# Kernel tuning notes

Measured on AMD Instinct MI355X. Metric: run time of the kernel, lower is better.

## Reference

```python
import jax, jax.numpy as jnp
import numpy as np

K = 8        # num capsules
DD = 64      # per-capsule dim (delta_d)
D = K * DD   # 512
T = 16384    # num target nodes (segments)
NB = 100000  # num neighbor nodes
E = 131072   # num edges
ROUIT = 3
BETA = 0.5


def seg_softmax(p, seg, num):
    # softmax over entries sharing the same segment id (axis 0)
    m = jax.lax.stop_gradient(jax.ops.segment_max(p, seg, num_segments=num))
    e = jnp.exp(p - m[seg])
    s = jax.ops.segment_sum(e, seg, num_segments=num)
    return e / s[seg]


def l2norm(x):
    # F.normalize along last axis with eps=1e-12
    n = jnp.sqrt(jnp.sum(x * x, axis=-1, keepdims=True))
    return x / jnp.maximum(n, 1e-12)


def setup_inputs() -> dict:
    key = jax.random.key(0)
    ks = jax.random.split(key, 9)
    return {
        "x_nb": jax.random.normal(ks[0], (NB, 512), dtype=jnp.float32),
        "ppr": jax.random.uniform(ks[1], (E,), dtype=jnp.float32),
        "pca_w": jax.random.normal(ks[2], (512, D), dtype=jnp.float32) * 0.02,
        "pca_b": jnp.zeros((D,), dtype=jnp.float32),
        "mlp_w": jax.random.normal(ks[3], (D, 40), dtype=jnp.float32) * 0.02,
        "mlp_b": jnp.zeros((40,), dtype=jnp.float32),
        "row_idx": jnp.sort(jax.random.randint(ks[4], (E,), 0, T, dtype=jnp.int32)),
        "col_idx": jax.random.randint(ks[5], (E,), 0, NB, dtype=jnp.int32),
        "x_idx": jax.random.randint(ks[6], (T,), 0, NB, dtype=jnp.int32),
    }


def reference(x_nb, ppr, pca_w, pca_b, mlp_w, mlp_b, row_idx, col_idx, x_idx):
    # pca projection + relu
    x = jax.nn.relu(x_nb @ pca_w + pca_b)            # (NB, D)
    # segment softmax of ppr over targets
    ppr = seg_softmax(ppr, row_idx, T)               # (E,)
    # is_xNorm: per-capsule l2 normalization
    x = l2norm(x.reshape(-1, K, DD)).reshape(-1, D)
    z = x[col_idx]                                   # (E, D) gathered neighbors
    zk = z.reshape(-1, K, DD)                        # (E, K, DD)
    # init_mtd == 2: ppr-weighted scatter-sum init
    u = jax.ops.segment_sum(z * ppr[:, None], row_idx, num_segments=T)  # (T, D)
    for it in range(ROUIT):
        uk = u[row_idx].reshape(-1, K, DD)           # (E, K, DD)
        p = jnp.einsum('ekd,ekd->ek', uk, zk)        # (E, K) capsule logits
        # attention == 1: segment softmax then blend with ppr
        p = seg_softmax(p, row_idx, T)
        p = BETA * p + (1.0 - BETA) * ppr[:, None]
        # final segment softmax
        p = seg_softmax(p, row_idx, T)
        u = jax.ops.segment_sum(zk * p[:, :, None], row_idx, num_segments=T)  # (T, K, DD)
        if it < ROUIT - 1:
            u = l2norm(u)
        u = u.reshape(T, D)
    out = jax.nn.relu(u)                             # dropout is identity at eval
    logits = out @ mlp_w + mlp_b                     # (T, nclass)
    return jax.nn.log_softmax(logits, axis=1)
```

## Files before the change

kernel.cpp:

```cpp
#include <hip/hip_runtime.h>
#include <cstdint>
#include <cstddef>

#define NB_N 100000
#define E_N  131072
#define T_N  16384
#define D_N  512
#define NCLS 40
#define NTILES 782
#define CAPR 12

typedef unsigned short u16;
typedef unsigned int   u32;
typedef __attribute__((ext_vector_type(8))) short  short8;
typedef __attribute__((ext_vector_type(4))) float  floatx4;

__device__ __forceinline__ u16 f2bf(float f) {
  u32 u = __float_as_uint(f);
  return (u16)((u + 0x7fffu + ((u >> 16) & 1u)) >> 16);
}
__device__ __forceinline__ void unpack8(uint4 z, float* f) {
  f[0] = __uint_as_float(z.x << 16);
  f[1] = __uint_as_float(z.x & 0xffff0000u);
  f[2] = __uint_as_float(z.y << 16);
  f[3] = __uint_as_float(z.y & 0xffff0000u);
  f[4] = __uint_as_float(z.z << 16);
  f[5] = __uint_as_float(z.z & 0xffff0000u);
  f[6] = __uint_as_float(z.w << 16);
  f[7] = __uint_as_float(z.w & 0xffff0000u);
}
__device__ __forceinline__ void gload_lds16(const void* g, void* s) {
  __builtin_amdgcn_global_load_lds(
      (const __attribute__((address_space(1))) unsigned int*)g,
      (__attribute__((address_space(3))) unsigned int*)s, 16, 0, 0);
}
__device__ __forceinline__ u32 cvtpk_bf16(float lo, float hi) {
  u32 r;
  asm("v_cvt_pk_bf16_f32 %0, %1, %2" : "=v"(r) : "v"(lo), "v"(hi));
  return r;
}

__global__ void conv_bt(const float* __restrict__ w, u16* __restrict__ Bt) {
  int i = blockIdx.x * 256 + threadIdx.x;
  int n = i >> 9, k = i & 511;
  Bt[i] = f2bf(w[k * 512 + n]);
}

__global__ void conv_bt2(const float* __restrict__ w, u16* __restrict__ Bt2) {
  int i = blockIdx.x * 256 + threadIdx.x;
  int n = i >> 9, k = i & 511;
  Bt2[i] = (n < NCLS) ? f2bf(w[k * NCLS + n]) : (u16)0;
}

__global__ void build_offs(const int* __restrict__ rowi, int* __restrict__ offs) {
  int e = blockIdx.x * 256 + threadIdx.x;
  if (e >= E_N) return;
  int r  = rowi[e];
  int rp = (e == 0) ? -1 : rowi[e - 1];
  for (int t = rp + 1; t <= r; ++t) offs[t] = e;
  if (e == E_N - 1)
    for (int t = r + 1; t <= T_N; ++t) offs[t] = E_N;
}

__global__ void ppr_sm(const float* __restrict__ ppr, const int* __restrict__ offs,
                       float* __restrict__ pprn) {
  int t = blockIdx.x * 256 + threadIdx.x;
  int s = offs[t], en = offs[t + 1];
  if (s >= en) return;
  float m = -INFINITY;
  for (int e = s; e < en; ++e) m = fmaxf(m, ppr[e]);
  float sum = 0.f;
  for (int e = s; e < en; ++e) sum += expf(ppr[e] - m);
  float inv = 1.f / sum;
  for (int e = s; e < en; ++e) pprn[e] = expf(ppr[e] - m) * inv;
}

__global__ __launch_bounds__(256, 2) void gemm_pca(
    const float* __restrict__ A,
    const u16*   __restrict__ Bt,
    const float* __restrict__ bias,
    u16*         __restrict__ xn) {
  __shared__ u16 SMEM[4 * 128 * 64];
  u16* As = SMEM;
  u16* Bs = SMEM + 16384;
  const int tid  = threadIdx.x;
  const int wid  = tid >> 6, lane = tid & 63;
  const int quad = lane >> 4, l16 = lane & 15;
  const int b  = blockIdx.x;
  const int mt = (b & 7) | ((b >> 5) << 3);
  if (mt >= NTILES) return;
  const int m0 = mt * 128;
  const int n0 = ((b >> 3) & 3) * 128;
  const int wm = (wid >> 1) * 64;
  const int wn = (wid & 1) * 64;
  const int sw = l16 & 7;

  floatx4 acc[4][4];
#pragma unroll
  for (int i = 0; i < 4; ++i)
#pragma unroll
    for (int j = 0; j < 4; ++j) acc[i][j] = (floatx4){0.f, 0.f, 0.f, 0.f};

  float4 pa0[4], pa1[4];

  auto issueA = [&](int k0) {
#pragma unroll
    for (int j = 0; j < 4; ++j) {
      int ci = j * 256 + tid;
      int row = ci >> 3, kc = ci & 7;
      int gm = m0 + row;
      if (gm > NB_N - 1) gm = NB_N - 1;
      const float* src = A + (size_t)gm * 512 + k0 + kc * 8;
      pa0[j] = *(const float4*)(src);
      pa1[j] = *(const float4*)(src + 4);
    }
  };
  auto writeA = [&](u16* dst) {
#pragma unroll
    for (int j = 0; j < 4; ++j) {
      int ci = j * 256 + tid;
      int row = ci >> 3, kc = ci & 7;
      uint4 pk;
      pk.x = cvtpk_bf16(pa0[j].x, pa0[j].y);
      pk.y = cvtpk_bf16(pa0[j].z, pa0[j].w);
      pk.z = cvtpk_bf16(pa1[j].x, pa1[j].y);
      pk.w = cvtpk_bf16(pa1[j].z, pa1[j].w);
      int dc = kc ^ (row & 7);
      *(uint4*)(&dst[(size_t)(row * 8 + dc) * 8]) = pk;
    }
  };
  auto issueB = [&](int k0, u16* dstB) {
#pragma unroll
    for (int j = 0; j < 4; ++j) {
      int ci  = j * 256 + wid * 64 + lane;
      int row = ci >> 3;
      int kcs = (lane & 7) ^ ((lane >> 3) & 7);
      gload_lds16(Bt + (size_t)(n0 + row) * 512 + k0 + kcs * 8,
                  &dstB[(size_t)(j * 256 + wid * 64) * 8]);
    }
  };

  issueA(0);
  issueB(0, Bs);
  writeA(As);
  issueA(64);
  asm volatile("s_waitcnt vmcnt(8) lgkmcnt(0)" ::: "memory");
  __builtin_amdgcn_s_barrier();
  __builtin_amdgcn_sched_barrier(0);

#pragma unroll
  for (int s = 0; s < 8; ++s) {
    const int cur = s & 1, nxt = cur ^ 1;
    const u16* Asc = As + cur * 8192;
    const u16* Bsc = Bs + cur * 8192;
    if (s + 1 < 8) issueB((s + 1) * 64, Bs + nxt * 8192);
#pragma unroll
    for (int kk = 0; kk < 64; kk += 32) {
      short8 af[4], bf[4];
#pragma unroll
      for (int mi = 0; mi < 4; ++mi) {
        int c = (kk >> 3) + quad;
        af[mi] = *(const short8*)(&Asc[(wm + mi * 16 + l16) * 64 + ((c ^ sw) << 3)]);
      }
#pragma unroll
      for (int ni = 0; ni < 4; ++ni) {
        int c = (kk >> 3) + quad;
        bf[ni] = *(const short8*)(&Bsc[(wn + ni * 16 + l16) * 64 + ((c ^ sw) << 3)]);
      }
#pragma unroll
      for (int mi = 0; mi < 4; ++mi)
#pragma unroll
        for (int ni = 0; ni < 4; ++ni)
          acc[mi][ni] = __builtin_amdgcn_mfma_f32_16x16x32_bf16(af[mi], bf[ni],
                                                                acc[mi][ni], 0, 0, 0);
    }
    if (s + 1 < 8) writeA(As + nxt * 8192);
    if (s + 2 < 8) issueA((s + 2) * 64);
    if (s + 1 < 8) {
      if (s + 2 < 8)
        asm volatile("s_waitcnt vmcnt(8) lgkmcnt(0)" ::: "memory");
      else
        asm volatile("s_waitcnt vmcnt(0) lgkmcnt(0)" ::: "memory");
      __builtin_amdgcn_s_barrier();
      __builtin_amdgcn_sched_barrier(0);
    }
  }
  __syncthreads();

  u16* Os = SMEM;
#pragma unroll
  for (int mi = 0; mi < 4; ++mi) {
#pragma unroll
    for (int r = 0; r < 4; ++r) {
      int lrow = wm + mi * 16 + quad * 4 + r;
      float v[4];
      float ss = 0.f;
#pragma unroll
      for (int ni = 0; ni < 4; ++ni) {
        int n  = n0 + wn + ni * 16 + l16;
        float x = acc[mi][ni][r] + bias[n];
        x = fmaxf(x, 0.f);
        v[ni] = x;
        ss += x * x;
      }
      ss += __shfl_xor(ss, 1);
      ss += __shfl_xor(ss, 2);
      ss += __shfl_xor(ss, 4);
      ss += __shfl_xor(ss, 8);
      float sc = 1.f / fmaxf(sqrtf(ss), 1e-12f);
#pragma unroll
      for (int ni = 0; ni < 4; ++ni)
        Os[lrow * 128 + wn + ni * 16 + l16] = f2bf(v[ni] * sc);
    }
  }
  __syncthreads();
#pragma unroll
  for (int c8 = 0; c8 < 8; ++c8) {
    int idx = c8 * 256 + tid;
    int row = idx >> 4, chk = idx & 15;
    int gm = m0 + row;
    if (gm < NB_N) {
      uint4 val = *(const uint4*)(&Os[row * 128 + chk * 8]);
      *(uint4*)(xn + (size_t)gm * 512 + n0 + chk * 8) = val;
    }
  }
}

__device__ __forceinline__ void matvec16(const float (&g0)[16], const float (&g1)[16],
                                         float w0, float w1, int base,
                                         float& e0, float& e1) {
  e0 = 0.f; e1 = 0.f;
#pragma unroll
  for (int j = 0; j < 8; ++j) {
    float wj = __shfl(w0, base | j);
    e0 += g0[j] * wj;
    e1 += g1[j] * wj;
  }
#pragma unroll
  for (int j = 0; j < 8; ++j) {
    float wj = __shfl(w1, base | j);
    e0 += g0[8 + j] * wj;
    e1 += g1[8 + j] * wj;
  }
}

__device__ __forceinline__ void segsm2(float& d0, float& d1, bool v0, bool v1) {
  float m = fmaxf(v0 ? d0 : -INFINITY, v1 ? d1 : -INFINITY);
  m = fmaxf(m, __shfl_xor(m, 1));
  m = fmaxf(m, __shfl_xor(m, 2));
  m = fmaxf(m, __shfl_xor(m, 4));
  float e0 = v0 ? expf(d0 - m) : 0.f;
  float e1 = v1 ? expf(d1 - m) : 0.f;
  float s = e0 + e1;
  s += __shfl_xor(s, 1);
  s += __shfl_xor(s, 2);
  s += __shfl_xor(s, 4);
  float inv = 1.f / s;
  d0 = e0 * inv;
  d1 = e1 * inv;
}

__global__ __launch_bounds__(128, 4) void fused_all(
    const u16* __restrict__ xn, const int* __restrict__ coli,
    const int* __restrict__ offs, const float* __restrict__ pprn,
    u16* __restrict__ ub) {
  __shared__ __align__(16) float Glds[2][8 * 260];
  const int lane = threadIdx.x & 63;
  const int wv = threadIdx.x >> 6;
  const int t = blockIdx.x * 2 + wv;
  const int s = offs[t], en = offs[t + 1];
  int deg = en - s;
  if (deg > 64) deg = 64;

  int   mycol = (lane < deg) ? coli[s + lane] : 0;
  float myppr = (lane < deg) ? pprn[s + lane] : 0.f;

  float uf[8] = {0.f, 0.f, 0.f, 0.f, 0.f, 0.f, 0.f, 0.f};

  if (deg <= 16) {
    float* G = Glds[wv];
    const int esrc = lane & 15, kq = lane >> 4;
    int ce = __shfl(mycol, esrc);
    const u16* zb = xn + (size_t)ce * 512 + kq * 8;
    floatx4 gram[8];
#pragma unroll
    for (int c = 0; c < 8; ++c) {
      short8 f0 = *(const short8*)(zb + c * 64);
      short8 f1 = *(const short8*)(zb + c * 64 + 32);
      floatx4 gg = (floatx4){0.f, 0.f, 0.f, 0.f};
      gg = __builtin_amdgcn_mfma_f32_16x16x32_bf16(f0, f0, gg, 0, 0, 0);
      gg = __builtin_amdgcn_mfma_f32_16x16x32_bf16(f1, f1, gg, 0, 0, 0);
      gram[c] = gg;
    }
#pragma unroll
    for (int c = 0; c < 8; ++c)
      *(float4*)&G[c * 260 + esrc * 16 + kq * 4] = *(float4*)&gram[c];
    const int cc = lane >> 3, i0 = lane & 7;
    const int base = lane & 56;
    float g0[16], g1[16];
    {
      const float* r0 = &G[cc * 260 + i0 * 16];
      const float* r1 = &G[cc * 260 + (i0 + 8) * 16];
#pragma unroll
      for (int ch = 0; ch < 4; ++ch) {
        float4 a = *(const float4*)(r0 + ch * 4);
        float4 b = *(const float4*)(r1 + ch * 4);
        g0[ch * 4 + 0] = a.x; g0[ch * 4 + 1] = a.y;
        g0[ch * 4 + 2] = a.z; g0[ch * 4 + 3] = a.w;
        g1[ch * 4 + 0] = b.x; g1[ch * 4 + 1] = b.y;
        g1[ch * 4 + 2] = b.z; g1[ch * 4 + 3] = b.w;
      }
    }
    const bool v0 = i0 < deg, v1 = (i0 + 8) < deg;
    float pr0 = __shfl(myppr, i0);
    float pr1 = __shfl(myppr, i0 + 8);

    float d0, d1;
    matvec16(g0, g1, pr0, pr1, base, d0, d1);

    float w0 = 0.f, w1 = 0.f;
#pragma unroll
    for (int it = 0; it < 3; ++it) {
      segsm2(d0, d1, v0, v1);
      d0 = 0.5f * d0 + 0.5f * pr0;
      d1 = 0.5f * d1 + 0.5f * pr1;
      segsm2(d0, d1, v0, v1);
      w0 = d0; w1 = d1;
      if (it < 2) {
        float e0, e1;
        matvec16(g0, g1, w0, w1, base, e0, e1);
        float nv = w0 * e0 + w1 * e1;
        nv += __shfl_xor(nv, 1);
        nv += __shfl_xor(nv, 2);
        nv += __shfl_xor(nv, 4);
        float invn = 1.f / fmaxf(sqrtf(nv), 1e-12f);
        d0 = e0 * invn;
        d1 = e1 * invn;
      }
    }

#pragma unroll
    for (int j = 0; j < 16; ++j) {
      if (j < deg) {
        float wj = __shfl((j < 8) ? w0 : w1, base | (j & 7));
        int cj = __shfl(mycol, j);
        uint4 zz = *(const uint4*)(xn + (size_t)cj * 512 + lane * 8);
        float zf[8];
        unpack8(zz, zf);
#pragma unroll
        for (int q = 0; q < 8; ++q) uf[q] += wj * zf[q];
      }
    }
  } else {
    const int cap = lane >> 3;
    const int slot = lane >> 3;

    uint4 zreg[CAPR];
#pragma unroll
    for (int j = 0; j < CAPR; ++j) {
      if (j < deg) {
        int c = __shfl(mycol, j);
        zreg[j] = *(const uint4*)(xn + (size_t)c * 512 + lane * 8);
      }
    }

#pragma unroll
    for (int j = 0; j < CAPR; ++j) {
      if (j < deg) {
        float w = __shfl(myppr, j);
        float zf[8];
        unpack8(zreg[j], zf);
#pragma unroll
        for (int q = 0; q < 8; ++q) uf[q] += w * zf[q];
      }
    }
    for (int j = CAPR; j < deg; ++j) {
      float w = __shfl(myppr, j);
      int c = __shfl(mycol, j);
      uint4 zz = *(const uint4*)(xn + (size_t)c * 512 + lane * 8);
      float zf[8];
      unpack8(zz, zf);
#pragma unroll
      for (int q = 0; q < 8; ++q) uf[q] += w * zf[q];
    }

    float Preg[8];

    for (int it = 0; it < 3; ++it) {
#pragma unroll
      for (int j = 0; j < CAPR; ++j) {
        if (j < deg) {
          float zf[8];
          unpack8(zreg[j], zf);
          float d = uf[0]*zf[0] + uf[1]*zf[1] + uf[2]*zf[2] + uf[3]*zf[3] +
                    uf[4]*zf[4] + uf[5]*zf[5] + uf[6]*zf[6] + uf[7]*zf[7];
          d += __shfl_xor(d, 1);
          d += __shfl_xor(d, 2);
          d += __shfl_xor(d, 4);
          float dc = __shfl(d, (lane & 7) << 3);
          if (slot == (j & 7)) Preg[j >> 3] = dc;
        }
      }
      for (int j = CAPR; j < deg; ++j) {
        int c = __shfl(mycol, j);
        uint4 zz = *(const uint4*)(xn + (size_t)c * 512 + lane * 8);
        float zf[8];
        unpack8(zz, zf);
        float d = uf[0]*zf[0] + uf[1]*zf[1] + uf[2]*zf[2] + uf[3]*zf[3] +
                  uf[4]*zf[4] + uf[5]*zf[5] + uf[6]*zf[6] + uf[7]*zf[7];
        d += __shfl_xor(d, 1);
        d += __shfl_xor(d, 2);
        d += __shfl_xor(d, 4);
        float dc = __shfl(d, (lane & 7) << 3);
        if (slot == (j & 7)) {
          int hi = j >> 3;
          if      (hi == 1) Preg[1] = dc;
          else if (hi == 2) Preg[2] = dc;
          else if (hi == 3) Preg[3] = dc;
          else if (hi == 4) Preg[4] = dc;
          else if (hi == 5) Preg[5] = dc;
          else if (hi == 6) Preg[6] = dc;
          else if (hi == 7) Preg[7] = dc;
        }
      }

      {
        float m1 = -INFINITY;
#pragma unroll
        for (int i = 0; i < 8; ++i)
          m1 = (slot + 8*i < deg) ? fmaxf(m1, Preg[i]) : m1;
        m1 = fmaxf(m1, __shfl_xor(m1, 8));
        m1 = fmaxf(m1, __shfl_xor(m1, 16));
        m1 = fmaxf(m1, __shfl_xor(m1, 32));
        float s1 = 0.f;
#pragma unroll
        for (int i = 0; i < 8; ++i)
          s1 += (slot + 8*i < deg) ? expf(Preg[i] - m1) : 0.f;
        s1 += __shfl_xor(s1, 8);
        s1 += __shfl_xor(s1, 16);
        s1 += __shfl_xor(s1, 32);
        float inv1 = 1.f / s1;
        float m2 = -INFINITY;
#pragma unroll
        for (int i = 0; i < 8; ++i) {
          int j = slot + 8*i;
          if (j < deg) {
            float pj = __shfl(myppr, j);
            float v = 0.5f * expf(Preg[i] - m1) * inv1 + 0.5f * pj;
            Preg[i] = v;
            m2 = fmaxf(m2, v);
          }
        }
        m2 = fmaxf(m2, __shfl_xor(m2, 8));
        m2 = fmaxf(m2, __shfl_xor(m2, 16));
        m2 = fmaxf(m2, __shfl_xor(m2, 32));
        float s2 = 0.f;
#pragma unroll
        for (int i = 0; i < 8; ++i)
          s2 += (slot + 8*i < deg) ? expf(Preg[i] - m2) : 0.f;
        s2 += __shfl_xor(s2, 8);
        s2 += __shfl_xor(s2, 16);
        s2 += __shfl_xor(s2, 32);
        float inv2 = 1.f / s2;
#pragma unroll
        for (int i = 0; i < 8; ++i)
          if (slot + 8*i < deg) Preg[i] = expf(Preg[i] - m2) * inv2;
      }

      float acc[8] = {0.f, 0.f, 0.f, 0.f, 0.f, 0.f, 0.f, 0.f};
#pragma unroll
      for (int j = 0; j < CAPR; ++j) {
        if (j < deg) {
          float w = __shfl(Preg[j >> 3], ((j & 7) << 3) | cap);
          float zf[8];
          unpack8(zreg[j], zf);
#pragma unroll
          for (int q = 0; q < 8; ++q) acc[q] += w * zf[q];
        }
      }
      for (int j = CAPR; j < deg; ++j) {
        int hi = j >> 3;
        float pr = Preg[1];
        if      (hi == 2) pr = Preg[2];
        else if (hi == 3) pr = Preg[3];
        else if (hi == 4) pr = Preg[4];
        else if (hi == 5) pr = Preg[5];
        else if (hi == 6) pr = Preg[6];
        else if (hi == 7) pr = Preg[7];
        float w = __shfl(pr, ((j & 7) << 3) | cap);
        int c = __shfl(mycol, j);
        uint4 zz = *(const uint4*)(xn + (size_t)c * 512 + lane * 8);
        float zf[8];
        unpack8(zz, zf);
#pragma unroll
        for (int q = 0; q < 8; ++q) acc[q] += w * zf[q];
      }
      if (it < 2) {
        float ss = 0.f;
#pragma unroll
        for (int q = 0; q < 8; ++q) ss += acc[q] * acc[q];
        ss += __shfl_xor(ss, 1);
        ss += __shfl_xor(ss, 2);
        ss += __shfl_xor(ss, 4);
        float sc = 1.f / fmaxf(sqrtf(ss), 1e-12f);
#pragma unroll
        for (int q = 0; q < 8; ++q) acc[q] *= sc;
      }
#pragma unroll
      for (int q = 0; q < 8; ++q) uf[q] = acc[q];
    }
  }

  uint4 pk;
  pk.x = (u32)f2bf(fmaxf(uf[0], 0.f)) | ((u32)f2bf(fmaxf(uf[1], 0.f)) << 16);
  pk.y = (u32)f2bf(fmaxf(uf[2], 0.f)) | ((u32)f2bf(fmaxf(uf[3], 0.f)) << 16);
  pk.z = (u32)f2bf(fmaxf(uf[4], 0.f)) | ((u32)f2bf(fmaxf(uf[5], 0.f)) << 16);
  pk.w = (u32)f2bf(fmaxf(uf[6], 0.f)) | ((u32)f2bf(fmaxf(uf[7], 0.f)) << 16);
  *(uint4*)(ub + (size_t)t * 512 + lane * 8) = pk;
}

__global__ __launch_bounds__(256) void mlp_gemm(
    const u16* __restrict__ ub, const u16* __restrict__ Bt2,
    const float* __restrict__ mb, float* __restrict__ out) {
  const int wid = threadIdx.x >> 6, lane = threadIdx.x & 63;
  const int quad = lane >> 4, l16 = lane & 15;
  const int m0 = blockIdx.x * 64 + wid * 16;

  floatx4 acc[4];
#pragma unroll
  for (int ni = 0; ni < 4; ++ni) acc[ni] = (floatx4){0.f, 0.f, 0.f, 0.f};

#pragma unroll 4
  for (int kk = 0; kk < 512; kk += 32) {
    short8 af = *(const short8*)(ub + (size_t)(m0 + l16) * 512 + kk + quad * 8);
#pragma unroll
    for (int ni = 0; ni < 4; ++ni) {
      short8 bf = *(const short8*)(Bt2 + (size_t)(ni * 16 + l16) * 512 + kk + quad * 8);
      acc[ni] = __builtin_amdgcn_mfma_f32_16x16x32_bf16(af, bf, acc[ni], 0, 0, 0);
    }
  }

#pragma unroll
  for (int r = 0; r < 4; ++r) {
    int t = m0 + quad * 4 + r;
    float v[4];
    float mx = -INFINITY;
#pragma unroll
    for (int ni = 0; ni < 4; ++ni) {
      int c = ni * 16 + l16;
      float lg = (c < NCLS) ? (acc[ni][r] + mb[c]) : -INFINITY;
      v[ni] = lg;
      mx = fmaxf(mx, lg);
    }
    mx = fmaxf(mx, __shfl_xor(mx, 1));
    mx = fmaxf(mx, __shfl_xor(mx, 2));
    mx = fmaxf(mx, __shfl_xor(mx, 4));
    mx = fmaxf(mx, __shfl_xor(mx, 8));
    float se = 0.f;
#pragma unroll
    for (int ni = 0; ni < 4; ++ni) {
      int c = ni * 16 + l16;
      if (c < NCLS) se += expf(v[ni] - mx);
    }
    se += __shfl_xor(se, 1);
    se += __shfl_xor(se, 2);
    se += __shfl_xor(se, 4);
    se += __shfl_xor(se, 8);
    float lse = mx + logf(se);
#pragma unroll
    for (int ni = 0; ni < 4; ++ni) {
      int c = ni * 16 + l16;
      if (c < NCLS) out[(size_t)t * NCLS + c] = v[ni] - lse;
    }
  }
}

extern "C" void kernel_launch(void* const* d_in, const int* in_sizes, int n_in,
                              void* d_out, int out_size, void* d_ws, size_t ws_size,
                              hipStream_t stream) {
  const float* x_nb  = (const float*)d_in[0];
  const float* ppr   = (const float*)d_in[1];
  const float* pca_w = (const float*)d_in[2];
  const float* pca_b = (const float*)d_in[3];
  const float* mlp_w = (const float*)d_in[4];
  const float* mlp_b = (const float*)d_in[5];
  const int* row_idx = (const int*)d_in[6];
  const int* col_idx = (const int*)d_in[7];
  float* out = (float*)d_out;

  char* ws = (char*)d_ws;
  const size_t OFF_BT   = 0;
  const size_t OFF_BT2  = 512 * 1024;
  const size_t OFF_PPRN = 640 * 1024;
  const size_t OFF_OFFS = 1152 * 1024;
  const size_t OFF_XN   = 1280 * 1024;
  const size_t OFF_UB   = OFF_XN + (size_t)NB_N * 512 * 2;
  u16*   Bt   = (u16*)(ws + OFF_BT);
  u16*   Bt2  = (u16*)(ws + OFF_BT2);
  float* pprn = (float*)(ws + OFF_PPRN);
  int*   offs = (int*)(ws + OFF_OFFS);
  u16*   xn   = (u16*)(ws + OFF_XN);
  u16*   ub   = (u16*)(ws + OFF_UB);

  conv_bt<<<1024, 256, 0, stream>>>(pca_w, Bt);
  conv_bt2<<<128, 256, 0, stream>>>(mlp_w, Bt2);
  build_offs<<<512, 256, 0, stream>>>(row_idx, offs);
  ppr_sm<<<64, 256, 0, stream>>>(ppr, offs, pprn);

  gemm_pca<<<98 * 32, 256, 0, stream>>>(x_nb, Bt, pca_b, xn);

  fused_all<<<T_N / 2, 128, 0, stream>>>(xn, col_idx, offs, pprn, ub);

  mlp_gemm<<<256, 256, 0, stream>>>(ub, Bt2, mlp_b, out);
}
```

Before: 473.9 us.

## Widen PCA GEMM tile to 128x256 with 512 threads and single-buffered A

The PCA GEMM block now covers 128 rows by 256 columns with eight waves instead of 128x128 with four. This halves the number of times each fp32 input row of x_nb is read and converted to bf16. The A tile in LDS becomes single-buffered and needs an extra barrier per k-step before it is overwritten, while B stays double-buffered. Launch bounds change to 512 threads with 4 blocks per CU, which tightens the register budget. The extra synchronisation may reduce overlap between loads and MFMA work.

```diff
diff --git a/kernel.cpp b/kernel.cpp
--- a/kernel.cpp
+++ b/kernel.cpp
@@ -75,24 +75,24 @@
   for (int e = s; e < en; ++e) pprn[e] = expf(ppr[e] - m) * inv;
 }
 
-__global__ __launch_bounds__(256, 2) void gemm_pca(
+__global__ __launch_bounds__(512, 4) void gemm_pca(
     const float* __restrict__ A,
     const u16*   __restrict__ Bt,
     const float* __restrict__ bias,
     u16*         __restrict__ xn) {
-  __shared__ u16 SMEM[4 * 128 * 64];
+  __shared__ u16 SMEM[40960];
   u16* As = SMEM;
-  u16* Bs = SMEM + 16384;
+  u16* Bs = SMEM + 8192;
   const int tid  = threadIdx.x;
   const int wid  = tid >> 6, lane = tid & 63;
   const int quad = lane >> 4, l16 = lane & 15;
   const int b  = blockIdx.x;
-  const int mt = (b & 7) | ((b >> 5) << 3);
+  const int mt = (b & 7) | ((b >> 4) << 3);
   if (mt >= NTILES) return;
   const int m0 = mt * 128;
-  const int n0 = ((b >> 3) & 3) * 128;
-  const int wm = (wid >> 1) * 64;
-  const int wn = (wid & 1) * 64;
+  const int n0 = ((b >> 3) & 1) * 256;
+  const int wm = (wid >> 2) * 64;
+  const int wn = (wid & 3) * 64;
   const int sw = l16 & 7;
 
   floatx4 acc[4][4];
@@ -101,66 +101,65 @@
 #pragma unroll
     for (int j = 0; j < 4; ++j) acc[i][j] = (floatx4){0.f, 0.f, 0.f, 0.f};
 
-  float4 pa0[4], pa1[4];
+  float4 pa[4];
 
   auto issueA = [&](int k0) {
 #pragma unroll
-    for (int j = 0; j < 4; ++j) {
-      int ci = j * 256 + tid;
+    for (int j = 0; j < 2; ++j) {
+      int ci = j * 512 + tid;
       int row = ci >> 3, kc = ci & 7;
       int gm = m0 + row;
       if (gm > NB_N - 1) gm = NB_N - 1;
       const float* src = A + (size_t)gm * 512 + k0 + kc * 8;
-      pa0[j] = *(const float4*)(src);
-      pa1[j] = *(const float4*)(src + 4);
+      pa[2 * j]     = *(const float4*)(src);
+      pa[2 * j + 1] = *(const float4*)(src + 4);
     }
   };
-  auto writeA = [&](u16* dst) {
-#pragma unroll
-    for (int j = 0; j < 4; ++j) {
-      int ci = j * 256 + tid;
+  auto writeA = [&]() {
+#pragma unroll
+    for (int j = 0; j < 2; ++j) {
+      int ci = j * 512 + tid;
       int row = ci >> 3, kc = ci & 7;
       uint4 pk;
-      pk.x = cvtpk_bf16(pa0[j].x, pa0[j].y);
-      pk.y = cvtpk_bf16(pa0[j].z, pa0[j].w);
-      pk.z = cvtpk_bf16(pa1[j].x, pa1[j].y);
-      pk.w = cvtpk_bf16(pa1[j].z, pa1[j].w);
+      pk.x = cvtpk_bf16(pa[2 * j].x, pa[2 * j].y);
+      pk.y = cvtpk_bf16(pa[2 * j].z, pa[2 * j].w);
+      pk.z = cvtpk_bf16(pa[2 * j + 1].x, pa[2 * j + 1].y);
+      pk.w = cvtpk_bf16(pa[2 * j + 1].z, pa[2 * j + 1].w);
       int dc = kc ^ (row & 7);
-      *(uint4*)(&dst[(size_t)(row * 8 + dc) * 8]) = pk;
+      *(uint4*)(&As[(size_t)(row * 8 + dc) * 8]) = pk;
     }
   };
   auto issueB = [&](int k0, u16* dstB) {
 #pragma unroll
     for (int j = 0; j < 4; ++j) {
-      int ci  = j * 256 + wid * 64 + lane;
+      int ci  = j * 512 + wid * 64 + lane;
       int row = ci >> 3;
       int kcs = (lane & 7) ^ ((lane >> 3) & 7);
       gload_lds16(Bt + (size_t)(n0 + row) * 512 + k0 + kcs * 8,
-                  &dstB[(size_t)(j * 256 + wid * 64) * 8]);
+                  &dstB[(size_t)(j * 512 + wid * 64) * 8]);
     }
   };
 
   issueA(0);
   issueB(0, Bs);
-  writeA(As);
+  writeA();
   issueA(64);
-  asm volatile("s_waitcnt vmcnt(8) lgkmcnt(0)" ::: "memory");
+  asm volatile("s_waitcnt vmcnt(4) lgkmcnt(0)" ::: "memory");
   __builtin_amdgcn_s_barrier();
   __builtin_amdgcn_sched_barrier(0);
 
 #pragma unroll
   for (int s = 0; s < 8; ++s) {
-    const int cur = s & 1, nxt = cur ^ 1;
-    const u16* Asc = As + cur * 8192;
-    const u16* Bsc = Bs + cur * 8192;
-    if (s + 1 < 8) issueB((s + 1) * 64, Bs + nxt * 8192);
+    const int cs = s & 1;
+    if (s + 1 < 8) issueB((s + 1) * 64, Bs + (cs ^ 1) * 16384);
+    const u16* Bsc = Bs + cs * 16384;
 #pragma unroll
     for (int kk = 0; kk < 64; kk += 32) {
       short8 af[4], bf[4];
 #pragma unroll
       for (int mi = 0; mi < 4; ++mi) {
         int c = (kk >> 3) + quad;
-        af[mi] = *(const short8*)(&Asc[(wm + mi * 16 + l16) * 64 + ((c ^ sw) << 3)]);
+        af[mi] = *(const short8*)(&As[(wm + mi * 16 + l16) * 64 + ((c ^ sw) << 3)]);
       }
 #pragma unroll
       for (int ni = 0; ni < 4; ++ni) {
@@ -174,13 +173,16 @@
           acc[mi][ni] = __builtin_amdgcn_mfma_f32_16x16x32_bf16(af[mi], bf[ni],
                                                                 acc[mi][ni], 0, 0, 0);
     }
-    if (s + 1 < 8) writeA(As + nxt * 8192);
-    if (s + 2 < 8) issueA((s + 2) * 64);
+    __builtin_amdgcn_s_barrier();
+    __builtin_amdgcn_sched_barrier(0);
     if (s + 1 < 8) {
-      if (s + 2 < 8)
-        asm volatile("s_waitcnt vmcnt(8) lgkmcnt(0)" ::: "memory");
-      else
+      writeA();
+      if (s + 2 < 8) {
+        issueA((s + 2) * 64);
+        asm volatile("s_waitcnt vmcnt(4) lgkmcnt(0)" ::: "memory");
+      } else {
         asm volatile("s_waitcnt vmcnt(0) lgkmcnt(0)" ::: "memory");
+      }
       __builtin_amdgcn_s_barrier();
       __builtin_amdgcn_sched_barrier(0);
     }
@@ -210,17 +212,17 @@
       float sc = 1.f / fmaxf(sqrtf(ss), 1e-12f);
 #pragma unroll
       for (int ni = 0; ni < 4; ++ni)
-        Os[lrow * 128 + wn + ni * 16 + l16] = f2bf(v[ni] * sc);
+        Os[lrow * 256 + wn + ni * 16 + l16] = f2bf(v[ni] * sc);
     }
   }
   __syncthreads();
 #pragma unroll
   for (int c8 = 0; c8 < 8; ++c8) {
-    int idx = c8 * 256 + tid;
-    int row = idx >> 4, chk = idx & 15;
+    int idx = c8 * 512 + tid;
+    int row = idx >> 5, chk = idx & 31;
     int gm = m0 + row;
     if (gm < NB_N) {
-      uint4 val = *(const uint4*)(&Os[row * 128 + chk * 8]);
+      uint4 val = *(const uint4*)(&Os[row * 256 + chk * 8]);
       *(uint4*)(xn + (size_t)gm * 512 + n0 + chk * 8) = val;
     }
   }
@@ -607,7 +609,7 @@
   build_offs<<<512, 256, 0, stream>>>(row_idx, offs);
   ppr_sm<<<64, 256, 0, stream>>>(ppr, offs, pprn);
 
-  gemm_pca<<<98 * 32, 256, 0, stream>>>(x_nb, Bt, pca_b, xn);
+  gemm_pca<<<98 * 16, 512, 0, stream>>>(x_nb, Bt, pca_b, xn);
 
   fused_all<<<T_N / 2, 128, 0, stream>>>(xn, col_idx, offs, pprn, ub);
 
```

Result: slower. 568.8 us (+20.0%).
